# Kernel optimization log

Measured on AMD Instinct MI355X. Metric: run time of the kernel, lower is better.

The kernel has to match this reference:

```python
import jax, jax.numpy as jnp
import numpy as np

ALPHA = 0.25
GAMMA = 2.0


def calc_iou(a, b):
    # a: [A,4] anchors, b: [M,4] gt boxes -> IoU [A,M]
    area = (b[:, 2] - b[:, 0]) * (b[:, 3] - b[:, 1])
    iw = jnp.clip(jnp.minimum(a[:, 2][:, None], b[:, 2]) - jnp.maximum(a[:, 0][:, None], b[:, 0]), 0.0)
    ih = jnp.clip(jnp.minimum(a[:, 3][:, None], b[:, 3]) - jnp.maximum(a[:, 1][:, None], b[:, 1]), 0.0)
    inter = iw * ih
    ua = jnp.clip(((a[:, 2] - a[:, 0]) * (a[:, 3] - a[:, 1]))[:, None] + area - inter, 1e-8)
    return inter / ua


def setup_inputs() -> dict:
    key = jax.random.key(0)
    k1, k2, k3, k4, k5, k6, k7, k8, k9 = jax.random.split(key, 9)
    B, A, M, C = 8, 100000, 64, 80
    # anchor grid: random centers over a 1024x1024 image, sizes 20..120
    cx = jax.random.uniform(k1, (A,)) * 1024.0
    cy = jax.random.uniform(k2, (A,)) * 1024.0
    w = jax.random.uniform(k3, (A,)) * 100.0 + 20.0
    h = jax.random.uniform(k4, (A,)) * 100.0 + 20.0
    anchors = jnp.stack([cx - 0.5 * w, cy - 0.5 * h, cx + 0.5 * w, cy + 0.5 * h], axis=1)[None]  # [1,A,4]
    classifications = jnp.clip(jax.random.uniform(k5, (B, A, C)), 1e-3, 1.0 - 1e-3)
    regressions = jax.random.normal(k6, (B, A, 4)) * 0.1
    # GT boxes = jittered copies of random anchors -> positive matches guaranteed
    idx = jax.random.randint(k7, (B, M), 0, A)
    boxes = anchors[0][idx] + jax.random.normal(k8, (B, M, 4)) * 2.0
    labels = jax.random.randint(k9, (B, M), 0, C).astype(jnp.float32)
    annotations = jnp.concatenate([boxes, labels[..., None]], axis=-1)  # [B,M,5]
    return {"classifications": classifications, "regressions": regressions,
            "anchors": anchors, "annotations": annotations,
            "pool_w": 32, "htr_gt_box": 0}


def reference(classifications, regressions, anchors, annotations, pool_w, htr_gt_box):
    anchor = anchors[0]                          # [A,4]
    aw = anchor[:, 2] - anchor[:, 0]
    ah = anchor[:, 3] - anchor[:, 1]
    acx = anchor[:, 0] + 0.5 * aw
    acy = anchor[:, 1] + 0.5 * ah
    std = jnp.array([0.1, 0.1, 0.2, 0.2], dtype=jnp.float32)
    num_classes = classifications.shape[-1]
    onehot0 = jnp.zeros((num_classes,), jnp.float32).at[0].set(1.0)  # assigned label forced to 0

    def per_sample(cls, reg, ann):
        cls = jnp.clip(cls, 1e-4, 1.0 - 1e-4)          # [A,C]
        iou = calc_iou(anchor, ann[:, :4])             # [A,M]
        iou_max = iou.max(axis=1)
        iou_arg = iou.argmax(axis=1)
        pos = iou_max >= 0.5
        neg = iou_max < 0.4
        # targets: +1 at class 0 for positives (label overwritten to 0), 0 for negatives, -1 ignore
        targets = jnp.where(pos[:, None], onehot0[None, :],
                            jnp.where(neg[:, None], 0.0, -1.0))  # [A,C]
        num_pos = pos.sum().astype(jnp.float32)
        alpha_factor = jnp.where(targets == 1.0, ALPHA, 1.0 - ALPHA)
        focal_w = alpha_factor * jnp.where(targets == 1.0, 1.0 - cls, cls) ** GAMMA
        bce = -(targets * jnp.log(cls) + (1.0 - targets) * jnp.log(1.0 - cls))
        cls_loss = jnp.where(targets != -1.0, focal_w * bce, 0.0).sum() / jnp.maximum(num_pos, 1.0)
        assigned = ann[iou_arg]                        # [A,5]
        gw = assigned[:, 2] - assigned[:, 0]
        gh = assigned[:, 3] - assigned[:, 1]
        gcx = assigned[:, 0] + 0.5 * gw
        gcy = assigned[:, 1] + 0.5 * gh
        gw = jnp.maximum(gw, 1.0)
        gh = jnp.maximum(gh, 1.0)
        t = jnp.stack([(gcx - acx) / aw, (gcy - acy) / ah,
                       jnp.log(gw / aw), jnp.log(gh / ah)], axis=1) / std  # [A,4]
        diff = jnp.abs(t - reg[:, :4])
        sl1 = jnp.where(diff <= 1.0 / 9.0, 0.5 * 9.0 * diff ** 2, diff - 0.5 / 9.0)
        reg_loss = jnp.where(num_pos > 0,
                             (sl1 * pos[:, None]).sum() / jnp.maximum(num_pos * 4.0, 1.0),
                             0.0)
        return cls_loss, reg_loss

    cl, rl = jax.vmap(per_sample)(classifications, regressions, annotations)
    return cl.mean(keepdims=True), rl.mean(keepdims=True)
```

## Files before the change

kernel.cpp:

```cpp
#include <hip/hip_runtime.h>

#define AN 100000
#define BN 8
#define MN 64
#define CN 80
#define NV4 (AN * CN / 4)
#define BLKX 391
#define NBLK (BLKX * BN)

#define NEGC (-0.5198603854199589f)
#define POSC (-0.1732867951399863f)


__global__ __launch_bounds__(256) void fused_kernel(
    const float4* __restrict__ anchors,
    const float4* __restrict__ regs,
    const float*  __restrict__ anns,
    const float4* __restrict__ cls4,
    const float*  __restrict__ cls,
    float4* __restrict__ partials)
{
    __shared__ float4 sbox[MN];
    __shared__ float  sarea[MN];
    __shared__ float  sw[256];
    const int tid    = threadIdx.x;
    const int b      = blockIdx.y;
    const int bx     = blockIdx.x;
    const int base_a = bx * 256;

    if (tid < MN) {
        const float* p = anns + ((size_t)b * MN + tid) * 5;
        float4 bb = make_float4(p[0], p[1], p[2], p[3]);
        sbox[tid]  = bb;
        sarea[tid] = (bb.z - bb.x) * (bb.w - bb.y);
    }
    __syncthreads();

    const int a = base_a + tid;
    float posf = 0.f, rsum = 0.f, corr = 0.f;
    float w = 0.f;
    if (a < AN) {
        const float4 an = anchors[a];
        const float ax1 = an.x, ay1 = an.y, ax2 = an.z, ay2 = an.w;
        const float aw = ax2 - ax1, ah = ay2 - ay1;
        const float aarea = aw * ah;

        float bestI = 0.f, bestU = 1.f;
        int   barg  = 0;
        #pragma unroll 16
        for (int m = 0; m < MN; ++m) {
            const float4 bb = sbox[m];
            float iw = fmaxf(fminf(ax2, bb.z) - fmaxf(ax1, bb.x), 0.f);
            float ih = fmaxf(fminf(ay2, bb.w) - fmaxf(ay1, bb.y), 0.f);
            float inter = iw * ih;
            float ua = fmaxf(aarea + sarea[m] - inter, 1e-8f);
            bool better = inter * bestU > bestI * ua;
            bestI = better ? inter : bestI;
            bestU = better ? ua    : bestU;
            barg  = better ? m     : barg;
        }

        const bool pos = bestI >= 0.5f * bestU;
        const bool ign = !pos && (bestI >= 0.4f * bestU);
        w = ign ? 0.f : NEGC;

        if (pos) {
            posf = 1.f;
            const float4 gb = sbox[barg];
            float gw = gb.z - gb.x, gh = gb.w - gb.y;
            float gcx = gb.x + 0.5f * gw, gcy = gb.y + 0.5f * gh;
            gw = fmaxf(gw, 1.f); gh = fmaxf(gh, 1.f);
            float acx = ax1 + 0.5f * aw, acy = ay1 + 0.5f * ah;
            float t0 = __fdividef(gcx - acx, aw) * 10.f;
            float t1 = __fdividef(gcy - acy, ah) * 10.f;
            float t2 = __logf(__fdividef(gw, aw)) * 5.f;
            float t3 = __logf(__fdividef(gh, ah)) * 5.f;
            const float4 rg = regs[(size_t)b * AN + a];
            float d0 = fabsf(t0 - rg.x), d1 = fabsf(t1 - rg.y);
            float d2 = fabsf(t2 - rg.z), d3 = fabsf(t3 - rg.w);
            const float TH = 1.f / 9.f, HB = 0.5f / 9.f;
            rsum  = (d0 <= TH ? 4.5f * d0 * d0 : d0 - HB);
            rsum += (d1 <= TH ? 4.5f * d1 * d1 : d1 - HB);
            rsum += (d2 <= TH ? 4.5f * d2 * d2 : d2 - HB);
            rsum += (d3 <= TH ? 4.5f * d3 * d3 : d3 - HB);
            float p0 = cls[((size_t)b * AN + a) * CN];
            corr = POSC * (1.f - p0) * (1.f - p0) * __log2f(p0)
                 - NEGC * p0 * p0 * __log2f(1.f - p0);
        }
    }
    sw[tid] = w;
    __syncthreads();

    const float4* __restrict__ cbase = cls4 + (size_t)b * NV4 + (size_t)base_a * 20;
    const bool tailblk = (base_a + 256 > AN);
    const int  ulim    = NV4 - base_a * 20 - 1;
    float acc = corr;
    #pragma unroll
    for (int i = 0; i < 20; ++i) {
        const int u  = i * 256 + tid;
        const int uu = tailblk ? min(u, ulim) : u;
        const float4 q = cbase[uu];
        const int al   = u / 20;
        const float m0 = q.x * q.x, L0 = __log2f(1.f - q.x);
        const float m1 = q.y * q.y, L1 = __log2f(1.f - q.y);
        const float m2 = q.z * q.z, L2 = __log2f(1.f - q.z);
        const float m3 = q.w * q.w, L3 = __log2f(1.f - q.w);
        const float t = m0 * L0 + m1 * L1 + m2 * L2 + m3 * L3;
        acc = fmaf(sw[al], t, acc);
    }

    float c = acc, r = rsum, p = posf;
    #pragma unroll
    for (int off = 32; off > 0; off >>= 1) {
        c += __shfl_down(c, off);
        r += __shfl_down(r, off);
        p += __shfl_down(p, off);
    }
    __shared__ float wc[4], wr[4], wp[4];
    const int wid = tid >> 6, lane = tid & 63;
    if (lane == 0) { wc[wid] = c; wr[wid] = r; wp[wid] = p; }
    __syncthreads();
    if (tid == 0) {
        partials[(size_t)b * BLKX + bx] =
            make_float4(wc[0] + wc[1] + wc[2] + wc[3],
                        wp[0] + wp[1] + wp[2] + wp[3],
                        wr[0] + wr[1] + wr[2] + wr[3], 0.f);
    }
}

__global__ __launch_bounds__(256) void finalize_kernel(
    const float4* __restrict__ partials, float* __restrict__ out)
{
    const int t = threadIdx.x;
    const int b = t >> 5;
    const int l = t & 31;
    double cs = 0.0;
    float  np = 0.f, rs = 0.f;
    for (int i = l; i < BLKX; i += 32) {
        const float4 q = partials[(size_t)b * BLKX + i];
        cs += (double)q.x; np += q.y; rs += q.z;
    }
    #pragma unroll
    for (int off = 16; off > 0; off >>= 1) {
        cs += __shfl_down(cs, off, 32);
        np += __shfl_down(np, off, 32);
        rs += __shfl_down(rs, off, 32);
    }
    __shared__ double scls[8];
    __shared__ float  snp[8], srs[8];
    if (l == 0) { scls[b] = cs; snp[b] = np; srs[b] = rs; }
    __syncthreads();
    if (t == 0) {
        double cacc = 0.0;
        float  racc = 0.f;
        #pragma unroll
        for (int i = 0; i < BN; ++i) {
            float npi = snp[i];
            cacc += scls[i] / (double)fmaxf(npi, 1.f);
            if (npi > 0.f) racc += srs[i] / (4.f * npi);
        }
        out[0] = (float)(cacc / (double)BN);
        out[1] = racc / (float)BN;
    }
}

extern "C" void kernel_launch(void* const* d_in, const int* in_sizes, int n_in,
                              void* d_out, int out_size, void* d_ws, size_t ws_size,
                              hipStream_t stream) {
    const float* cls     = (const float*)d_in[0];
    const float* regs    = (const float*)d_in[1];
    const float* anchors = (const float*)d_in[2];
    const float* anns    = (const float*)d_in[3];
    float* out = (float*)d_out;

    float4* partials = (float4*)d_ws;

    dim3 grid(BLKX, BN);
    fused_kernel<<<grid, 256, 0, stream>>>((const float4*)anchors,
                                           (const float4*)regs,
                                           anns,
                                           (const float4*)cls,
                                           cls,
                                           partials);

    finalize_kernel<<<1, 256, 0, stream>>>(partials, out);
}
```

Baseline: 55.63 us.

## Prefetch classification tiles before IoU matching and use nontemporal loads

Issues the first eight float4 classification loads per thread before the IoU/anchor-matching phase, so their memory latency overlaps with that compute. The remaining loads are staged in batches of eight and four, interleaved with the focal-loss arithmetic. All streaming loads now use nontemporal load builtins to avoid polluting cache. The cost is higher register pressure (up to 16 float4 live), which may reduce occupancy.

Result: no change. 56.61 us (+1.8%).

```diff
diff --git a/kernel.cpp b/kernel.cpp
--- a/kernel.cpp
+++ b/kernel.cpp
@@ -10,6 +10,13 @@
 
 #define NEGC (-0.5198603854199589f)
 #define POSC (-0.1732867951399863f)
+
+typedef float f32x4 __attribute__((ext_vector_type(4)));
+
+__device__ __forceinline__ float4 ldnt(const float4* p) {
+    f32x4 v = __builtin_nontemporal_load((const f32x4*)p);
+    return make_float4(v.x, v.y, v.z, v.w);
+}
 
 
 __global__ __launch_bounds__(256) void fused_kernel(
@@ -34,6 +41,17 @@
         sbox[tid]  = bb;
         sarea[tid] = (bb.z - bb.x) * (bb.w - bb.y);
     }
+
+    const float4* __restrict__ cbase = cls4 + (size_t)b * NV4 + (size_t)base_a * 20;
+    const bool tailblk = (base_a + 256 > AN);
+    const int  ulim    = NV4 - base_a * 20 - 1;
+    float4 qa[8], qb[8];
+    #pragma unroll
+    for (int i = 0; i < 8; ++i) {
+        const int u = i * 256 + tid;
+        qa[i] = ldnt(cbase + (tailblk ? min(u, ulim) : u));
+    }
+
     __syncthreads();
 
     const int a = base_a + tid;
@@ -91,21 +109,49 @@
     sw[tid] = w;
     __syncthreads();
 
-    const float4* __restrict__ cbase = cls4 + (size_t)b * NV4 + (size_t)base_a * 20;
-    const bool tailblk = (base_a + 256 > AN);
-    const int  ulim    = NV4 - base_a * 20 - 1;
     float acc = corr;
-    #pragma unroll
-    for (int i = 0; i < 20; ++i) {
+
+    #pragma unroll
+    for (int i = 0; i < 8; ++i) {
+        const int u = (i + 8) * 256 + tid;
+        qb[i] = ldnt(cbase + (tailblk ? min(u, ulim) : u));
+    }
+    #pragma unroll
+    for (int i = 0; i < 8; ++i) {
         const int u  = i * 256 + tid;
-        const int uu = tailblk ? min(u, ulim) : u;
-        const float4 q = cbase[uu];
-        const int al   = u / 20;
-        const float m0 = q.x * q.x, L0 = __log2f(1.f - q.x);
-        const float m1 = q.y * q.y, L1 = __log2f(1.f - q.y);
-        const float m2 = q.z * q.z, L2 = __log2f(1.f - q.z);
-        const float m3 = q.w * q.w, L3 = __log2f(1.f - q.w);
-        const float t = m0 * L0 + m1 * L1 + m2 * L2 + m3 * L3;
+        const int al = u / 20;
+        const float4 q = qa[i];
+        const float t = q.x * q.x * __log2f(1.f - q.x)
+                      + q.y * q.y * __log2f(1.f - q.y)
+                      + q.z * q.z * __log2f(1.f - q.z)
+                      + q.w * q.w * __log2f(1.f - q.w);
+        acc = fmaf(sw[al], t, acc);
+    }
+    #pragma unroll
+    for (int i = 0; i < 4; ++i) {
+        const int u = (i + 16) * 256 + tid;
+        qa[i] = ldnt(cbase + (tailblk ? min(u, ulim) : u));
+    }
+    #pragma unroll
+    for (int i = 0; i < 8; ++i) {
+        const int u  = (i + 8) * 256 + tid;
+        const int al = u / 20;
+        const float4 q = qb[i];
+        const float t = q.x * q.x * __log2f(1.f - q.x)
+                      + q.y * q.y * __log2f(1.f - q.y)
+                      + q.z * q.z * __log2f(1.f - q.z)
+                      + q.w * q.w * __log2f(1.f - q.w);
+        acc = fmaf(sw[al], t, acc);
+    }
+    #pragma unroll
+    for (int i = 0; i < 4; ++i) {
+        const int u  = (i + 16) * 256 + tid;
+        const int al = u / 20;
+        const float4 q = qa[i];
+        const float t = q.x * q.x * __log2f(1.f - q.x)
+                      + q.y * q.y * __log2f(1.f - q.y)
+                      + q.z * q.z * __log2f(1.f - q.z)
+                      + q.w * q.w * __log2f(1.f - q.w);
         acc = fmaf(sw[al], t, acc);
     }
 
```

## Split IoU argmax across thread pairs and halve anchors per block

Applied to the files above, without the earlier changes.

Each block now covers 128 anchors instead of 256. Two threads share each anchor and each scans half of the 64 GT boxes, then the pair merges its best IoU with a lane shuffle. This halves the serial IoU loop per thread and doubles the grid size, which should give more parallelism and better overlap of the compute phase with the streaming loads of the class scores. The cost is twice as many blocks, each redoing the shared-memory box setup, twice as many partials to reduce, and half of the threads idle in the positive-anchor branch.

Result: no change. 55.04 us (-1.1%).

```diff
diff --git a/kernel.cpp b/kernel.cpp
--- a/kernel.cpp
+++ b/kernel.cpp
@@ -5,7 +5,8 @@
 #define MN 64
 #define CN 80
 #define NV4 (AN * CN / 4)
-#define BLKX 391
+#define APB 128
+#define BLKX 782
 #define NBLK (BLKX * BN)
 
 #define NEGC (-0.5198603854199589f)
@@ -22,11 +23,11 @@
 {
     __shared__ float4 sbox[MN];
     __shared__ float  sarea[MN];
-    __shared__ float  sw[256];
+    __shared__ float  sw[APB];
     const int tid    = threadIdx.x;
     const int b      = blockIdx.y;
     const int bx     = blockIdx.x;
-    const int base_a = bx * 256;
+    const int base_a = bx * APB;
 
     if (tid < MN) {
         const float* p = anns + ((size_t)b * MN + tid) * 5;
@@ -36,7 +37,9 @@
     }
     __syncthreads();
 
-    const int a = base_a + tid;
+    const int aidx = tid >> 1;
+    const int half = tid & 1;
+    const int a    = base_a + aidx;
     float posf = 0.f, rsum = 0.f, corr = 0.f;
     float w = 0.f;
     if (a < AN) {
@@ -46,9 +49,11 @@
         const float aarea = aw * ah;
 
         float bestI = 0.f, bestU = 1.f;
-        int   barg  = 0;
+        int   barg  = half * 32;
+        const int mbase = half * 32;
         #pragma unroll 16
-        for (int m = 0; m < MN; ++m) {
+        for (int mm = 0; mm < 32; ++mm) {
+            const int m = mbase + mm;
             const float4 bb = sbox[m];
             float iw = fmaxf(fminf(ax2, bb.z) - fmaxf(ax1, bb.x), 0.f);
             float ih = fmaxf(fminf(ay2, bb.w) - fmaxf(ay1, bb.y), 0.f);
@@ -59,14 +64,24 @@
             bestU = better ? ua    : bestU;
             barg  = better ? m     : barg;
         }
-
-        const bool pos = bestI >= 0.5f * bestU;
-        const bool ign = !pos && (bestI >= 0.4f * bestU);
+        const float oI = __shfl_xor(bestI, 1);
+        const float oU = __shfl_xor(bestU, 1);
+        const int   og = __shfl_xor(barg, 1);
+        const float I0 = half ? oI : bestI, U0 = half ? oU : bestU;
+        const float I1 = half ? bestI : oI, U1 = half ? bestU : oU;
+        const int   g0 = half ? og : barg,  g1 = half ? barg : og;
+        const bool  b1 = I1 * U0 > I0 * U1;
+        const float bI = b1 ? I1 : I0;
+        const float bU = b1 ? U1 : U0;
+        const int   bg = b1 ? g1 : g0;
+
+        const bool pos = bI >= 0.5f * bU;
+        const bool ign = !pos && (bI >= 0.4f * bU);
         w = ign ? 0.f : NEGC;
 
-        if (pos) {
+        if (half == 0 && pos) {
             posf = 1.f;
-            const float4 gb = sbox[barg];
+            const float4 gb = sbox[bg];
             float gw = gb.z - gb.x, gh = gb.w - gb.y;
             float gcx = gb.x + 0.5f * gw, gcy = gb.y + 0.5f * gh;
             gw = fmaxf(gw, 1.f); gh = fmaxf(gh, 1.f);
@@ -88,15 +103,15 @@
                  - NEGC * p0 * p0 * __log2f(1.f - p0);
         }
     }
-    sw[tid] = w;
+    if (half == 0) sw[aidx] = w;
     __syncthreads();
 
     const float4* __restrict__ cbase = cls4 + (size_t)b * NV4 + (size_t)base_a * 20;
-    const bool tailblk = (base_a + 256 > AN);
+    const bool tailblk = (base_a + APB > AN);
     const int  ulim    = NV4 - base_a * 20 - 1;
     float acc = corr;
     #pragma unroll
-    for (int i = 0; i < 20; ++i) {
+    for (int i = 0; i < 10; ++i) {
         const int u  = i * 256 + tid;
         const int uu = tailblk ? min(u, ulim) : u;
         const float4 q = cbase[uu];
```
